# Performance work log

Hardware: AMD Instinct MI355X
Metric: run time of the kernel (lower is better)

Reference implementation:

```python
import jax, jax.numpy as jnp
import numpy as np

D_MODEL = 768
NUM_HEADS = 12
HEAD_DIM = D_MODEL // NUM_HEADS
THETA = 10000.0
SEQ = 4096
BATCH = 2


def setup_inputs() -> dict:
    key = jax.random.key(0)
    ks = jax.random.split(key, 5)
    std = np.sqrt(2.0 / (D_MODEL + D_MODEL)).astype(np.float32)
    x = jax.random.normal(ks[0], (BATCH, SEQ, D_MODEL), dtype=jnp.float32)
    token_positions = jnp.arange(SEQ, dtype=jnp.int32)
    # Linear stores weight as (d_out, d_in), applied as x @ W.T
    wq = jax.random.normal(ks[1], (D_MODEL, D_MODEL), dtype=jnp.float32) * std
    wk = jax.random.normal(ks[2], (D_MODEL, D_MODEL), dtype=jnp.float32) * std
    wv = jax.random.normal(ks[3], (D_MODEL, D_MODEL), dtype=jnp.float32) * std
    wo = jax.random.normal(ks[4], (D_MODEL, D_MODEL), dtype=jnp.float32) * std
    return {"x": x, "token_positions": token_positions,
            "wq": wq, "wk": wk, "wv": wv, "wo": wo}


def _apply_rope(t, positions):
    # t: [B, H, S, hd], positions: [S]
    half = HEAD_DIM // 2
    inv_freq = THETA ** (-jnp.arange(0, HEAD_DIM, 2, dtype=jnp.float32) / HEAD_DIM)  # [half]
    angles = positions.astype(jnp.float32)[:, None] * inv_freq  # [S, half]
    cos = jnp.repeat(jnp.cos(angles), 2, axis=-1)  # [S, hd]
    sin = jnp.repeat(jnp.sin(angles), 2, axis=-1)  # [S, hd]
    # rotate pairs: (-x1, x0, -x3, x2, ...)
    t2 = jnp.stack([-t[..., 1::2], t[..., ::2]], axis=-1).reshape(t.shape)
    return t * cos + t2 * sin


def reference(x, token_positions, wq, wk, wv, wo):
    B, S, D = x.shape
    H, hd = NUM_HEADS, HEAD_DIM
    q = (x @ wq.T).reshape(B, S, H, hd).transpose(0, 2, 1, 3)  # [B,H,S,hd]
    k = (x @ wk.T).reshape(B, S, H, hd).transpose(0, 2, 1, 3)
    v = (x @ wv.T).reshape(B, S, H, hd).transpose(0, 2, 1, 3)
    q = _apply_rope(q, token_positions)
    k = _apply_rope(k, token_positions)
    scale = hd ** -0.5
    scores = jnp.einsum('bhqd,bhkd->bhqk', q, k) * scale  # [B,H,S,S]
    causal = jnp.tril(jnp.ones((S, S), dtype=bool))
    scores = jnp.where(causal, scores, -jnp.inf)
    att = jax.nn.softmax(scores, axis=-1)
    out = jnp.einsum('bhqk,bhkd->bhqd', att, v)  # [B,H,S,hd]
    out = out.transpose(0, 2, 1, 3).reshape(B, S, D)
    return out @ wo.T
```

## Files before the change

### kernel.cpp

```cpp
#include <hip/hip_runtime.h>
#include <hip/hip_bf16.h>
#include <stdint.h>

#define D_MODEL 768
#define NHEADS 12
#define HD 64
#define SEQ 4096
#define BATCH 2
#define MTOT (BATCH*SEQ)
#define BHN (BATCH*NHEADS)

typedef __attribute__((ext_vector_type(8))) short short8;
typedef __attribute__((ext_vector_type(4))) float f32x4;
typedef __attribute__((ext_vector_type(16))) float f32x16;
typedef __attribute__((ext_vector_type(4))) int i32x4;

__device__ inline unsigned short f2bf(float f) {
  union { float f; unsigned u; } v; v.f = f;
  unsigned r = (v.u + 0x7FFFu + ((v.u >> 16) & 1u)) >> 16;
  return (unsigned short)r;
}
__device__ inline unsigned cvtpk_bf16(float lo, float hi) {
  unsigned r;
  asm("v_cvt_pk_bf16_f32 %0, %1, %2" : "=v"(r) : "v"(lo), "v"(hi));
  return r;
}
__device__ inline void perm32swap(unsigned &a, unsigned &b) {
  asm("v_permlane32_swap_b32 %0, %1" : "+v"(a), "+v"(b));
}
__device__ inline float exp2fast(float x) {
  float r;
  asm("v_exp_f32 %0, %1" : "=v"(r) : "v"(x));
  return r;
}
__device__ inline void gload16(const void* g, void* l) {
  __builtin_amdgcn_global_load_lds(
      (const __attribute__((address_space(1))) unsigned int*)g,
      (__attribute__((address_space(3))) unsigned int*)l, 16, 0, 0);
}

__global__ void k_conv(const float* __restrict__ x,  const float* __restrict__ wq,
                       const float* __restrict__ wk, const float* __restrict__ wv,
                       const float* __restrict__ wo,
                       unsigned short* __restrict__ xb,  unsigned short* __restrict__ wqb,
                       unsigned short* __restrict__ wkb, unsigned short* __restrict__ wvb,
                       unsigned short* __restrict__ wob)
{
  int i = blockIdx.x * blockDim.x + threadIdx.x;
  const int X4 = MTOT*D_MODEL/4;
  const int W4 = D_MODEL*D_MODEL/4;
  const float* src; unsigned short* dst; int idx;
  if (i < X4) { src = x; dst = xb; idx = i; }
  else {
    int j = i - X4;
    if      (j <   W4) { src = wq; dst = wqb; idx = j; }
    else if (j < 2*W4) { src = wk; dst = wkb; idx = j -   W4; }
    else if (j < 3*W4) { src = wv; dst = wvb; idx = j - 2*W4; }
    else if (j < 4*W4) { src = wo; dst = wob; idx = j - 3*W4; }
    else return;
  }
  float4 v = ((const float4*)src)[idx];
  ushort4 o;
  o.x = f2bf(v.x); o.y = f2bf(v.y); o.z = f2bf(v.z); o.w = f2bf(v.w);
  ((ushort4*)dst)[idx] = o;
}

__global__ void k_ropetab(const int* __restrict__ pos, float* __restrict__ ct, float* __restrict__ st) {
  int i = blockIdx.x * blockDim.x + threadIdx.x;
  if (i >= SEQ*32) return;
  int s = i & (SEQ-1), j = i >> 12;
  float p = (float)pos[s];
  const float L = 0.2878231366242557f;
  float freq = __expf(-L * (float)j);
  float a = p * freq;
  ct[i] = cosf(a);
  st[i] = sinf(a);
}

__global__ __launch_bounds__(256)
void k_gemm_qkv(const unsigned short* __restrict__ X,
                const unsigned short* __restrict__ Wq,
                const unsigned short* __restrict__ Wk,
                const unsigned short* __restrict__ Wv,
                unsigned short* __restrict__ Qp,
                unsigned short* __restrict__ Kp,
                unsigned short* __restrict__ VT,
                const float* __restrict__ ct,
                const float* __restrict__ st)
{
  __shared__ __align__(16) unsigned short As[2][128*32];
  __shared__ __align__(16) unsigned short Bs[2][128*32];
  const int tid = threadIdx.x;
  const int wave = tid >> 6, lane = tid & 63;
  const int lr = lane & 15, lg = lane >> 4;
  const int wr = wave >> 1, wc = wave & 1;
  const int m0 = blockIdx.x * 128;
  const int n0 = blockIdx.y * 128;
  const int z  = blockIdx.z;
  const unsigned short* B = (z == 0) ? Wq : (z == 1) ? Wk : Wv;
  const int K = 768;

  f32x4 acc[4][4] = {};
  const int srow = tid >> 2, scol = (tid & 3) << 3;
  const unsigned short* ag = X + (size_t)(m0 + srow) * K + scol;
  const unsigned short* bg = B + (size_t)(n0 + srow) * K + scol;

  {
    char* a0 = (char*)As[0] + wave*1024;
    char* a1 = (char*)As[0] + 4096 + wave*1024;
    char* b0 = (char*)Bs[0] + wave*1024;
    char* b1 = (char*)Bs[0] + 4096 + wave*1024;
    gload16(ag, a0);
    gload16(ag + (size_t)64*K, a1);
    gload16(bg, b0);
    gload16(bg + (size_t)64*K, b1);
  }
  int cur = 0;
  for (int k0 = 0; k0 < K; k0 += 32) {
    __syncthreads();
    if (k0 + 32 < K) {
      char* a0 = (char*)As[cur^1] + wave*1024;
      char* a1 = (char*)As[cur^1] + 4096 + wave*1024;
      char* b0 = (char*)Bs[cur^1] + wave*1024;
      char* b1 = (char*)Bs[cur^1] + 4096 + wave*1024;
      gload16(ag + k0 + 32, a0);
      gload16(ag + (size_t)64*K + k0 + 32, a1);
      gload16(bg + k0 + 32, b0);
      gload16(bg + (size_t)64*K + k0 + 32, b1);
    }
    short8 af[4], bfr[4];
    #pragma unroll
    for (int i = 0; i < 4; ++i)
      af[i] = *(const short8*)&As[cur][(wr*64 + i*16 + lr)*32 + lg*8];
    #pragma unroll
    for (int j = 0; j < 4; ++j)
      bfr[j] = *(const short8*)&Bs[cur][(wc*64 + j*16 + lr)*32 + lg*8];
    #pragma unroll
    for (int i = 0; i < 4; ++i)
      #pragma unroll
      for (int j = 0; j < 4; ++j)
        acc[i][j] = __builtin_amdgcn_mfma_f32_16x16x32_bf16(af[i], bfr[j], acc[i][j], 0, 0, 0);
    cur ^= 1;
  }

  #pragma unroll
  for (int i = 0; i < 4; ++i)
    #pragma unroll
    for (int j = 0; j < 4; ++j) {
      const int n = n0 + wc*64 + j*16 + lr;
      const int h = n >> 6, d = n & (HD-1);
      if (z == 2) {
        #pragma unroll
        for (int r = 0; r < 4; ++r) {
          int m = m0 + wr*64 + i*16 + lg*4 + r;
          int bb = m >> 12, s = m & (SEQ-1);
          VT[(((size_t)bb*NHEADS + h)*HD + d)*SEQ + s] = f2bf(acc[i][j][r]);
        }
      } else {
        unsigned short* dst = (z == 0) ? Qp : Kp;
        const int jrow = d >> 1;
        const int mb = m0 + wr*64 + i*16 + lg*4;
        const int bb = mb >> 12;
        const int sbase = mb & (SEQ-1);
        f32x4 cs4 = *(const f32x4*)(ct + (size_t)jrow*SEQ + sbase);
        f32x4 sn4 = *(const f32x4*)(st + (size_t)jrow*SEQ + sbase);
        #pragma unroll
        for (int r = 0; r < 4; ++r) {
          float vv = acc[i][j][r];
          float pp = __shfl_xor(vv, 1);
          float res = (d & 1) ? (vv*cs4[r] + pp*sn4[r]) : (vv*cs4[r] - pp*sn4[r]);
          if (z == 0) res *= 0.18033688011112043f;
          dst[(((size_t)bb*NHEADS + h)*SEQ + (sbase + r))*HD + d] = f2bf(res);
        }
      }
    }
}

__global__ __launch_bounds__(256)
void k_gemm_wo(const unsigned short* __restrict__ X,
               const unsigned short* __restrict__ W,
               float* __restrict__ out)
{
  __shared__ __align__(16) unsigned short As[2][128*32];
  __shared__ __align__(16) unsigned short Bs[2][128*32];
  const int tid = threadIdx.x;
  const int wave = tid >> 6, lane = tid & 63;
  const int lr = lane & 15, lg = lane >> 4;
  const int wr = wave >> 1, wc = wave & 1;
  const int m0 = blockIdx.x * 128;
  const int n0 = blockIdx.y * 128;
  const int K = 768;

  f32x4 acc[4][4] = {};
  const int srow = tid >> 2, scol = (tid & 3) << 3;
  const unsigned short* ag = X + (size_t)(m0 + srow) * K + scol;
  const unsigned short* bg = W + (size_t)(n0 + srow) * K + scol;

  {
    char* a0 = (char*)As[0] + wave*1024;
    char* a1 = (char*)As[0] + 4096 + wave*1024;
    char* b0 = (char*)Bs[0] + wave*1024;
    char* b1 = (char*)Bs[0] + 4096 + wave*1024;
    gload16(ag, a0);
    gload16(ag + (size_t)64*K, a1);
    gload16(bg, b0);
    gload16(bg + (size_t)64*K, b1);
  }
  int cur = 0;
  for (int k0 = 0; k0 < K; k0 += 32) {
    __syncthreads();
    if (k0 + 32 < K) {
      char* a0 = (char*)As[cur^1] + wave*1024;
      char* a1 = (char*)As[cur^1] + 4096 + wave*1024;
      char* b0 = (char*)Bs[cur^1] + wave*1024;
      char* b1 = (char*)Bs[cur^1] + 4096 + wave*1024;
      gload16(ag + k0 + 32, a0);
      gload16(ag + (size_t)64*K + k0 + 32, a1);
      gload16(bg + k0 + 32, b0);
      gload16(bg + (size_t)64*K + k0 + 32, b1);
    }
    short8 af[4], bfr[4];
    #pragma unroll
    for (int i = 0; i < 4; ++i)
      af[i] = *(const short8*)&As[cur][(wr*64 + i*16 + lr)*32 + lg*8];
    #pragma unroll
    for (int j = 0; j < 4; ++j)
      bfr[j] = *(const short8*)&Bs[cur][(wc*64 + j*16 + lr)*32 + lg*8];
    #pragma unroll
    for (int i = 0; i < 4; ++i)
      #pragma unroll
      for (int j = 0; j < 4; ++j)
        acc[i][j] = __builtin_amdgcn_mfma_f32_16x16x32_bf16(af[i], bfr[j], acc[i][j], 0, 0, 0);
    cur ^= 1;
  }

  #pragma unroll
  for (int i = 0; i < 4; ++i)
    #pragma unroll
    for (int j = 0; j < 4; ++j)
      #pragma unroll
      for (int r = 0; r < 4; ++r) {
        int m = m0 + wr*64 + i*16 + lg*4 + r;
        int n = n0 + wc*64 + j*16 + lr;
        out[(size_t)m*D_MODEL + n] = acc[i][j][r];
      }
}

__global__ __launch_bounds__(256, 3)
void k_attn(const unsigned short* __restrict__ Qp,
            const unsigned short* __restrict__ Kp,
            const unsigned short* __restrict__ VT,
            unsigned short* __restrict__ AO)
{
  __shared__ __align__(16) unsigned short Ks[2][64*64];
  __shared__ __align__(16) unsigned short Vs[2][64*64];

  const int tid = threadIdx.x;
  const int wave = tid >> 6, lane = tid & 63;
  const int qcol = lane & 31, hi = lane >> 5;

  const int u = blockIdx.x;
  const int kk = u >> 8, g = u & 255;
  const int rank = (kk == 0) ? g : (kk == 1) ? (767 - g) : (256 + g);
  const int cpair = rank / 24;
  const int bh = rank - cpair * 24;

  const int b = bh / NHEADS, h = bh % NHEADS;
  const int chunk = (wave < 2) ? cpair : 63 - cpair;
  const int qw = chunk * 64 + (wave & 1) * 32;
  const int nt = 64 - cpair;
  const int myNt = qw / 64 + 1;

  const unsigned short* Qh = Qp + (size_t)bh * SEQ * HD;
  const unsigned short* Kh = Kp + (size_t)bh * SEQ * HD;
  const unsigned short* Vh = VT + (size_t)bh * HD * SEQ;

  short8 qf[4];
  #pragma unroll
  for (int ds = 0; ds < 4; ++ds)
    qf[ds] = *(const short8*)(Qh + (size_t)(qw + qcol)*HD + ds*16 + hi*8);

  short8 onesf;
  #pragma unroll
  for (int i = 0; i < 8; ++i) onesf[i] = (short)0x3F80;

  f32x16 o[2] = {};
  f32x16 lacc = {};

  const int g_row = tid >> 3;
  const int sgp = ((tid & 7) ^ (g_row & 7)) * 8;

  {
    gload16(Kh + (size_t)g_row*HD + sgp,          (char*)Ks[0] + wave*1024);
    gload16(Kh + (size_t)(g_row + 32)*HD + sgp,   (char*)Ks[0] + 4096 + wave*1024);
    gload16(Vh + (size_t)g_row*SEQ + sgp,         (char*)Vs[0] + wave*1024);
    gload16(Vh + (size_t)(g_row + 32)*SEQ + sgp,  (char*)Vs[0] + 4096 + wave*1024);
  }
  __syncthreads();

  int cur = 0;
  for (int kt = 0; kt < nt; ++kt) {
    if (kt + 1 < nt) {
      const size_t kb = (size_t)(kt + 1) * 64;
      gload16(Kh + (kb + g_row)*HD + sgp,            (char*)Ks[cur^1] + wave*1024);
      gload16(Kh + (kb + g_row + 32)*HD + sgp,       (char*)Ks[cur^1] + 4096 + wave*1024);
      gload16(Vh + (size_t)g_row*SEQ + kb + sgp,     (char*)Vs[cur^1] + wave*1024);
      gload16(Vh + (size_t)(g_row + 32)*SEQ + kb + sgp, (char*)Vs[cur^1] + 4096 + wave*1024);
    }
    if (kt < myNt) {
      const char* Kb = (const char*)Ks[cur];
      const char* Vb = (const char*)Vs[cur];
      f32x16 c[2];
      __builtin_amdgcn_s_setprio(1);
      #pragma unroll
      for (int kc = 0; kc < 2; ++kc) {
        f32x16 acc = {};
        #pragma unroll
        for (int ds = 0; ds < 4; ++ds) {
          const int row = kc*32 + qcol;
          short8 kf = *(const short8*)(Kb + row*128 + ((ds*32 + hi*16) ^ ((row & 7) << 4)));
          acc = __builtin_amdgcn_mfma_f32_32x32x16_bf16(kf, qf[ds], acc, 0, 0, 0);
        }
        c[kc] = acc;
      }
      __builtin_amdgcn_s_setprio(0);
      if (kt == myNt - 1) {
        const int q = qw + qcol;
        #pragma unroll
        for (int kc = 0; kc < 2; ++kc)
          #pragma unroll
          for (int r = 0; r < 16; ++r) {
            int key = kt*64 + kc*32 + (r & 3) + 8*(r >> 2) + 4*hi;
            if (key > q) c[kc][r] = -1e30f;
          }
      }
      #pragma unroll
      for (int kc = 0; kc < 2; ++kc)
        #pragma unroll
        for (int r = 0; r < 16; ++r)
          c[kc][r] = exp2fast(c[kc][r]);
      unsigned U[8][2];
      #pragma unroll
      for (int g2 = 0; g2 < 8; ++g2) {
        const int fc = g2 >> 2, gq = g2 & 3;
        U[g2][0] = cvtpk_bf16(c[fc][4*gq + 0], c[fc][4*gq + 1]);
        U[g2][1] = cvtpk_bf16(c[fc][4*gq + 2], c[fc][4*gq + 3]);
      }
      #pragma unroll
      for (int ks = 0; ks < 4; ++ks) {
        unsigned j0 = U[2*ks][0], j2 = U[2*ks+1][0];
        perm32swap(j0, j2);
        unsigned j1 = U[2*ks][1], j3 = U[2*ks+1][1];
        perm32swap(j1, j3);
        union { unsigned u[4]; short8 s; } pf;
        pf.u[0] = j0; pf.u[1] = j1; pf.u[2] = j2; pf.u[3] = j3;
        __builtin_amdgcn_s_setprio(1);
        #pragma unroll
        for (int dc = 0; dc < 2; ++dc) {
          const int row = dc*32 + qcol;
          short8 vf = *(const short8*)(Vb + row*128 + ((ks*32 + hi*16) ^ ((row & 7) << 4)));
          o[dc] = __builtin_amdgcn_mfma_f32_32x32x16_bf16(vf, pf.s, o[dc], 0, 0, 0);
        }
        lacc = __builtin_amdgcn_mfma_f32_32x32x16_bf16(onesf, pf.s, lacc, 0, 0, 0);
        __builtin_amdgcn_s_setprio(0);
      }
    }
    __syncthreads();
    cur ^= 1;
  }

  const float inv = 1.0f / lacc[0];
  const size_t rowbase = ((size_t)b*SEQ + qw + qcol) * D_MODEL + h*HD;
  #pragma unroll
  for (int dc = 0; dc < 2; ++dc)
    #pragma unroll
    for (int g2 = 0; g2 < 4; ++g2) {
      ushort4 pk;
      pk.x = f2bf(o[dc][4*g2 + 0] * inv);
      pk.y = f2bf(o[dc][4*g2 + 1] * inv);
      pk.z = f2bf(o[dc][4*g2 + 2] * inv);
      pk.w = f2bf(o[dc][4*g2 + 3] * inv);
      const int d0 = dc*32 + 8*g2 + 4*hi;
      *(ushort4*)(AO + rowbase + d0) = pk;
    }
}

extern "C" void kernel_launch(void* const* d_in, const int* in_sizes, int n_in,
                              void* d_out, int out_size, void* d_ws, size_t ws_size,
                              hipStream_t stream)
{
  const float* x  = (const float*)d_in[0];
  const int* posi = (const int*)d_in[1];
  const float* wq = (const float*)d_in[2];
  const float* wk = (const float*)d_in[3];
  const float* wv = (const float*)d_in[4];
  const float* wo = (const float*)d_in[5];
  float* out = (float*)d_out;

  char* ws = (char*)d_ws;
  size_t off = 0;
  auto alloc = [&](size_t bytes) {
    char* p = ws + off;
    off += (bytes + 255) & ~(size_t)255;
    return p;
  };
  unsigned short* xb  = (unsigned short*)alloc((size_t)MTOT*D_MODEL*2);
  unsigned short* wqb = (unsigned short*)alloc((size_t)D_MODEL*D_MODEL*2);
  unsigned short* wkb = (unsigned short*)alloc((size_t)D_MODEL*D_MODEL*2);
  unsigned short* wvb = (unsigned short*)alloc((size_t)D_MODEL*D_MODEL*2);
  unsigned short* wob = (unsigned short*)alloc((size_t)D_MODEL*D_MODEL*2);
  unsigned short* Qb  = (unsigned short*)alloc((size_t)BHN*SEQ*HD*2);
  unsigned short* Kb  = (unsigned short*)alloc((size_t)BHN*SEQ*HD*2);
  unsigned short* VTb = (unsigned short*)alloc((size_t)BHN*HD*SEQ*2);
  unsigned short* AOb = (unsigned short*)alloc((size_t)MTOT*D_MODEL*2);
  float* ct = (float*)alloc((size_t)SEQ*32*4);
  float* st = (float*)alloc((size_t)SEQ*32*4);

  const int total4 = MTOT*D_MODEL/4 + 4*(D_MODEL*D_MODEL/4);
  k_conv<<<(total4 + 255)/256, 256, 0, stream>>>(x, wq, wk, wv, wo, xb, wqb, wkb, wvb, wob);
  k_ropetab<<<(SEQ*32 + 255)/256, 256, 0, stream>>>(posi, ct, st);

  k_gemm_qkv<<<dim3(MTOT/128, D_MODEL/128, 3), 256, 0, stream>>>(xb, wqb, wkb, wvb, Qb, Kb, VTb, ct, st);
  k_attn<<<dim3(768), 256, 0, stream>>>(Qb, Kb, VTb, AOb);
  k_gemm_wo<<<dim3(MTOT/128, D_MODEL/128), 256, 0, stream>>>(AOb, wob, out);
}
```

Measured before the change: 167.9 us.

## Triple-buffer K/V tiles in attention with prefetch distance two and partial vmcnt waits

The attention kernel's K/V shared-memory staging goes from two buffers to three. Loads are now issued two tiles ahead, and each iteration waits only for the older batch of loads (vmcnt(4)) instead of draining everything through __syncthreads. This is meant to hide more global-load latency behind the MFMA work. In exchange, LDS use grows from 32KB to 48KB per block, which may cut occupancy under launch_bounds(256,3). The raw s_barrier also relies on the vmcnt accounting being exact.

Result: no change. 168.4 us (+0.3%).

```diff
diff --git a/kernel.cpp b/kernel.cpp
--- a/kernel.cpp
+++ b/kernel.cpp
@@ -252,8 +252,8 @@
             const unsigned short* __restrict__ VT,
             unsigned short* __restrict__ AO)
 {
-  __shared__ __align__(16) unsigned short Ks[2][64*64];
-  __shared__ __align__(16) unsigned short Vs[2][64*64];
+  __shared__ __align__(16) unsigned short Ks[3][64*64];
+  __shared__ __align__(16) unsigned short Vs[3][64*64];
 
   const int tid = threadIdx.x;
   const int wave = tid >> 6, lane = tid & 63;
@@ -290,26 +290,27 @@
   const int g_row = tid >> 3;
   const int sgp = ((tid & 7) ^ (g_row & 7)) * 8;
 
-  {
-    gload16(Kh + (size_t)g_row*HD + sgp,          (char*)Ks[0] + wave*1024);
-    gload16(Kh + (size_t)(g_row + 32)*HD + sgp,   (char*)Ks[0] + 4096 + wave*1024);
-    gload16(Vh + (size_t)g_row*SEQ + sgp,         (char*)Vs[0] + wave*1024);
-    gload16(Vh + (size_t)(g_row + 32)*SEQ + sgp,  (char*)Vs[0] + 4096 + wave*1024);
-  }
-  __syncthreads();
-
-  int cur = 0;
+  auto STAGE = [&](int t, int bi) {
+    const size_t kb = (size_t)t * 64;
+    gload16(Kh + (kb + g_row)*HD + sgp,               (char*)Ks[bi] + wave*1024);
+    gload16(Kh + (kb + g_row + 32)*HD + sgp,          (char*)Ks[bi] + 4096 + wave*1024);
+    gload16(Vh + (size_t)g_row*SEQ + kb + sgp,        (char*)Vs[bi] + wave*1024);
+    gload16(Vh + (size_t)(g_row + 32)*SEQ + kb + sgp, (char*)Vs[bi] + 4096 + wave*1024);
+  };
+
+  STAGE(0, 0);
+  if (nt > 1) STAGE(1, 1);
+  if (nt > 1) { asm volatile("s_waitcnt vmcnt(4)" ::: "memory"); }
+  else        { asm volatile("s_waitcnt vmcnt(0)" ::: "memory"); }
+  __builtin_amdgcn_s_barrier();
+
+  int bc = 0, bn = 1, bs = 2;
   for (int kt = 0; kt < nt; ++kt) {
-    if (kt + 1 < nt) {
-      const size_t kb = (size_t)(kt + 1) * 64;
-      gload16(Kh + (kb + g_row)*HD + sgp,            (char*)Ks[cur^1] + wave*1024);
-      gload16(Kh + (kb + g_row + 32)*HD + sgp,       (char*)Ks[cur^1] + 4096 + wave*1024);
-      gload16(Vh + (size_t)g_row*SEQ + kb + sgp,     (char*)Vs[cur^1] + wave*1024);
-      gload16(Vh + (size_t)(g_row + 32)*SEQ + kb + sgp, (char*)Vs[cur^1] + 4096 + wave*1024);
-    }
+    const bool issue = (kt + 2 < nt);
+    if (issue) STAGE(kt + 2, bs);
     if (kt < myNt) {
-      const char* Kb = (const char*)Ks[cur];
-      const char* Vb = (const char*)Vs[cur];
+      const char* Kb = (const char*)Ks[bc];
+      const char* Vb = (const char*)Vs[bc];
       f32x16 c[2];
       __builtin_amdgcn_s_setprio(1);
       #pragma unroll
@@ -365,8 +366,10 @@
         __builtin_amdgcn_s_setprio(0);
       }
     }
-    __syncthreads();
-    cur ^= 1;
+    if (issue) { asm volatile("s_waitcnt vmcnt(4)" ::: "memory"); }
+    else       { asm volatile("s_waitcnt vmcnt(0)" ::: "memory"); }
+    __builtin_amdgcn_s_barrier();
+    const int t = bc; bc = bn; bn = bs; bs = t;
   }
 
   const float inv = 1.0f / lacc[0];
```

## Split paired attention blocks into single-chunk 128-thread blocks with reversed scheduling

Applied to the files above, without the earlier changes.

The attention kernel previously paired a short and a long causal query chunk in one 256-thread block, so both pairs of waves streamed the full key range while the short-chunk waves idled. Each 2-wave block now handles one 64-row query chunk and loads only the keys it needs. The grid doubles to 1536 blocks, ordered longest-first with a serpentine pattern for load balance. Staging K/V tiles now takes four loads each per thread instead of two, and smaller blocks mean more blocks and more barriers per CU.

After: 167.4 us. Within noise of the previous version (-0.3%).

```diff
diff --git a/kernel.cpp b/kernel.cpp
--- a/kernel.cpp
+++ b/kernel.cpp
@@ -246,7 +246,7 @@
       }
 }
 
-__global__ __launch_bounds__(256, 3)
+__global__ __launch_bounds__(128, 3)
 void k_attn(const unsigned short* __restrict__ Qp,
             const unsigned short* __restrict__ Kp,
             const unsigned short* __restrict__ VT,
@@ -261,15 +261,13 @@
 
   const int u = blockIdx.x;
   const int kk = u >> 8, g = u & 255;
-  const int rank = (kk == 0) ? g : (kk == 1) ? (767 - g) : (256 + g);
-  const int cpair = rank / 24;
-  const int bh = rank - cpair * 24;
+  const int rank = (kk & 1) ? ((kk + 1) * 256 - 1 - g) : (kk * 256 + g);
+  const int chunk = 63 - rank / 24;
+  const int bh = rank % 24;
 
   const int b = bh / NHEADS, h = bh % NHEADS;
-  const int chunk = (wave < 2) ? cpair : 63 - cpair;
-  const int qw = chunk * 64 + (wave & 1) * 32;
-  const int nt = 64 - cpair;
-  const int myNt = qw / 64 + 1;
+  const int qw = chunk * 64 + wave * 32;
+  const int nt = chunk + 1;
 
   const unsigned short* Qh = Qp + (size_t)bh * SEQ * HD;
   const unsigned short* Kh = Kp + (size_t)bh * SEQ * HD;
@@ -290,80 +288,77 @@
   const int g_row = tid >> 3;
   const int sgp = ((tid & 7) ^ (g_row & 7)) * 8;
 
-  {
-    gload16(Kh + (size_t)g_row*HD + sgp,          (char*)Ks[0] + wave*1024);
-    gload16(Kh + (size_t)(g_row + 32)*HD + sgp,   (char*)Ks[0] + 4096 + wave*1024);
-    gload16(Vh + (size_t)g_row*SEQ + sgp,         (char*)Vs[0] + wave*1024);
-    gload16(Vh + (size_t)(g_row + 32)*SEQ + sgp,  (char*)Vs[0] + 4096 + wave*1024);
-  }
+  auto STAGE = [&](int t, int bi) {
+    const size_t kb = (size_t)t * 64;
+    #pragma unroll
+    for (int bp = 0; bp < 4; ++bp) {
+      const int row = bp*16 + g_row;
+      gload16(Kh + (kb + row)*HD + sgp,            (char*)Ks[bi] + bp*2048 + wave*1024);
+      gload16(Vh + (size_t)row*SEQ + kb + sgp,     (char*)Vs[bi] + bp*2048 + wave*1024);
+    }
+  };
+
+  STAGE(0, 0);
   __syncthreads();
 
   int cur = 0;
   for (int kt = 0; kt < nt; ++kt) {
-    if (kt + 1 < nt) {
-      const size_t kb = (size_t)(kt + 1) * 64;
-      gload16(Kh + (kb + g_row)*HD + sgp,            (char*)Ks[cur^1] + wave*1024);
-      gload16(Kh + (kb + g_row + 32)*HD + sgp,       (char*)Ks[cur^1] + 4096 + wave*1024);
-      gload16(Vh + (size_t)g_row*SEQ + kb + sgp,     (char*)Vs[cur^1] + wave*1024);
-      gload16(Vh + (size_t)(g_row + 32)*SEQ + kb + sgp, (char*)Vs[cur^1] + 4096 + wave*1024);
-    }
-    if (kt < myNt) {
-      const char* Kb = (const char*)Ks[cur];
-      const char* Vb = (const char*)Vs[cur];
-      f32x16 c[2];
-      __builtin_amdgcn_s_setprio(1);
-      #pragma unroll
-      for (int kc = 0; kc < 2; ++kc) {
-        f32x16 acc = {};
-        #pragma unroll
-        for (int ds = 0; ds < 4; ++ds) {
-          const int row = kc*32 + qcol;
-          short8 kf = *(const short8*)(Kb + row*128 + ((ds*32 + hi*16) ^ ((row & 7) << 4)));
-          acc = __builtin_amdgcn_mfma_f32_32x32x16_bf16(kf, qf[ds], acc, 0, 0, 0);
-        }
-        c[kc] = acc;
+    if (kt + 1 < nt) STAGE(kt + 1, cur ^ 1);
+    const char* Kb = (const char*)Ks[cur];
+    const char* Vb = (const char*)Vs[cur];
+    f32x16 c[2];
+    __builtin_amdgcn_s_setprio(1);
+    #pragma unroll
+    for (int kc = 0; kc < 2; ++kc) {
+      f32x16 acc = {};
+      #pragma unroll
+      for (int ds = 0; ds < 4; ++ds) {
+        const int row = kc*32 + qcol;
+        short8 kf = *(const short8*)(Kb + row*128 + ((ds*32 + hi*16) ^ ((row & 7) << 4)));
+        acc = __builtin_amdgcn_mfma_f32_32x32x16_bf16(kf, qf[ds], acc, 0, 0, 0);
       }
-      __builtin_amdgcn_s_setprio(0);
-      if (kt == myNt - 1) {
-        const int q = qw + qcol;
-        #pragma unroll
-        for (int kc = 0; kc < 2; ++kc)
-          #pragma unroll
-          for (int r = 0; r < 16; ++r) {
-            int key = kt*64 + kc*32 + (r & 3) + 8*(r >> 2) + 4*hi;
-            if (key > q) c[kc][r] = -1e30f;
-          }
-      }
+      c[kc] = acc;
+    }
+    __builtin_amdgcn_s_setprio(0);
+    if (kt == nt - 1) {
+      const int q = qw + qcol;
       #pragma unroll
       for (int kc = 0; kc < 2; ++kc)
         #pragma unroll
-        for (int r = 0; r < 16; ++r)
-          c[kc][r] = exp2fast(c[kc][r]);
-      unsigned U[8][2];
-      #pragma unroll
-      for (int g2 = 0; g2 < 8; ++g2) {
-        const int fc = g2 >> 2, gq = g2 & 3;
-        U[g2][0] = cvtpk_bf16(c[fc][4*gq + 0], c[fc][4*gq + 1]);
-        U[g2][1] = cvtpk_bf16(c[fc][4*gq + 2], c[fc][4*gq + 3]);
+        for (int r = 0; r < 16; ++r) {
+          int key = kt*64 + kc*32 + (r & 3) + 8*(r >> 2) + 4*hi;
+          if (key > q) c[kc][r] = -1e30f;
+        }
+    }
+    #pragma unroll
+    for (int kc = 0; kc < 2; ++kc)
+      #pragma unroll
+      for (int r = 0; r < 16; ++r)
+        c[kc][r] = exp2fast(c[kc][r]);
+    unsigned U[8][2];
+    #pragma unroll
+    for (int g2 = 0; g2 < 8; ++g2) {
+      const int fc = g2 >> 2, gq = g2 & 3;
+      U[g2][0] = cvtpk_bf16(c[fc][4*gq + 0], c[fc][4*gq + 1]);
+      U[g2][1] = cvtpk_bf16(c[fc][4*gq + 2], c[fc][4*gq + 3]);
+    }
+    #pragma unroll
+    for (int ks = 0; ks < 4; ++ks) {
+      unsigned j0 = U[2*ks][0], j2 = U[2*ks+1][0];
+      perm32swap(j0, j2);
+      unsigned j1 = U[2*ks][1], j3 = U[2*ks+1][1];
+      perm32swap(j1, j3);
+      union { unsigned u[4]; short8 s; } pf;
+      pf.u[0] = j0; pf.u[1] = j1; pf.u[2] = j2; pf.u[3] = j3;
+      __builtin_amdgcn_s_setprio(1);
+      #pragma unroll
+      for (int dc = 0; dc < 2; ++dc) {
+        const int row = dc*32 + qcol;
+        short8 vf = *(const short8*)(Vb + row*128 + ((ks*32 + hi*16) ^ ((row & 7) << 4)));
+        o[dc] = __builtin_amdgcn_mfma_f32_32x32x16_bf16(vf, pf.s, o[dc], 0, 0, 0);
       }
-      #pragma unroll
-      for (int ks = 0; ks < 4; ++ks) {
-        unsigned j0 = U[2*ks][0], j2 = U[2*ks+1][0];
-        perm32swap(j0, j2);
-        unsigned j1 = U[2*ks][1], j3 = U[2*ks+1][1];
-        perm32swap(j1, j3);
-        union { unsigned u[4]; short8 s; } pf;
-        pf.u[0] = j0; pf.u[1] = j1; pf.u[2] = j2; pf.u[3] = j3;
-        __builtin_amdgcn_s_setprio(1);
-        #pragma unroll
-        for (int dc = 0; dc < 2; ++dc) {
-          const int row = dc*32 + qcol;
-          short8 vf = *(const short8*)(Vb + row*128 + ((ks*32 + hi*16) ^ ((row & 7) << 4)));
-          o[dc] = __builtin_amdgcn_mfma_f32_32x32x16_bf16(vf, pf.s, o[dc], 0, 0, 0);
-        }
-        lacc = __builtin_amdgcn_mfma_f32_32x32x16_bf16(onesf, pf.s, lacc, 0, 0, 0);
-        __builtin_amdgcn_s_setprio(0);
-      }
+      lacc = __builtin_amdgcn_mfma_f32_32x32x16_bf16(onesf, pf.s, lacc, 0, 0, 0);
+      __builtin_amdgcn_s_setprio(0);
     }
     __syncthreads();
     cur ^= 1;
@@ -421,6 +416,6 @@
   k_ropetab<<<(SEQ*32 + 255)/256, 256, 0, stream>>>(posi, ct, st);
 
   k_gemm_qkv<<<dim3(MTOT/128, D_MODEL/128, 3), 256, 0, stream>>>(xb, wqb, wkb, wvb, Qb, Kb, VTb, ct, st);
-  k_attn<<<dim3(768), 256, 0, stream>>>(Qb, Kb, VTb, AOb);
+  k_attn<<<dim3(1536), 128, 0, stream>>>(Qb, Kb, VTb, AOb);
   k_gemm_wo<<<dim3(MTOT/128, D_MODEL/128), 256, 0, stream>>>(AOb, wob, out);
 }
```
